# Kernel tuning notes

Hardware: AMD Instinct MI355X
Metric: run time of the kernel (lower is better)

The kernel has to match this reference:

```python
import jax, jax.numpy as jnp
import numpy as np

TAU = 1.0
EPS = 1e-8  # torch cosine_similarity norm clamp


def setup_inputs() -> dict:
    key = jax.random.key(0)
    k1, k2, k3 = jax.random.split(key, 3)
    B, d, M, C = 4096, 128, 8192, 16
    f = jax.random.normal(k1, (B, d), dtype=jnp.float32)
    f_neg = jax.random.normal(k2, (M, d), dtype=jnp.float32)
    labels = jax.random.randint(k3, (B,), 0, C, dtype=jnp.int64)
    return {"f": f, "f_neg": f_neg, "labels": labels, "batch_size": B}


def _normalize(x):
    n = jnp.linalg.norm(x, axis=-1, keepdims=True)
    return x / jnp.maximum(n, EPS)


def reference(f, f_neg, labels, batch_size):
    B = batch_size
    fn = _normalize(f)            # [B, d]
    gn = _normalize(f_neg)        # [M, d]

    sim_bb = jnp.einsum('id,jd->ij', fn, fn)   # [B, B] cosine sims in-batch
    sim_bn = jnp.einsum('id,md->im', fn, gn)   # [B, M] sims with neg bank

    offdiag = ~jnp.eye(B, dtype=bool)                       # exclude self
    pos_mask = (labels[:, None] == labels[None, :]) & offdiag  # [B, B]

    exp_bb = jnp.exp(sim_bb / TAU) * offdiag                # self row removed
    exp_bn = jnp.exp(sim_bn / TAU)
    # denominator_i = sum over all non-self in-batch + all bank negatives
    denom = exp_bb.sum(axis=1) + exp_bn.sum(axis=1)         # [B]

    # -log(exp(s_p/tau)/denom) = log(denom) - s_p/tau, averaged over positives
    neg_log = jnp.log(denom)[:, None] - sim_bb / TAU        # [B, B]
    n_pos = pos_mask.sum(axis=1)                            # [B]
    loss_i = jnp.sum(jnp.where(pos_mask, neg_log, 0.0), axis=1) / n_pos

    return jnp.sum(loss_i) / B  # reduction='mean'
```

## Files before the change

kernel.cpp:

```cpp
#include <hip/hip_runtime.h>
#include <hip/hip_bf16.h>
#include <hip/hip_fp8.h>

#define B_ROWS 4096
#define D_K    128
#define M_ROWS 8192
#define N_TOT  12288
#define NCHUNK 32
#define JT_PER_CHUNK 6
#define JCOLS  64
#define NCLS   16
#define NSTRIPE 32

typedef __attribute__((ext_vector_type(4))) int   intx4;
typedef __attribute__((ext_vector_type(8))) int   intx8;
typedef __attribute__((ext_vector_type(4))) float floatx4;

__device__ __forceinline__ float fp8_to_f32(unsigned char b) {
    __hip_fp8_e4m3 h; h.__x = b; return float(h);
}

__global__ __launch_bounds__(256) void nrm_kernel(
    const float* __restrict__ f, const float* __restrict__ fneg,
    unsigned char* __restrict__ G8, unsigned char* __restrict__ A8,
    float* __restrict__ selfdot, float* __restrict__ expself,
    float* __restrict__ out)
{
    const int tid  = threadIdx.x;
    const int wave = tid >> 6;
    const int lane = tid & 63;
    const int row  = blockIdx.x * 4 + wave;
    if (blockIdx.x == 0 && tid == 0) out[0] = 0.f;
    const float* src = (row < B_ROWS) ? (f + (size_t)row * D_K)
                                      : (fneg + (size_t)(row - B_ROWS) * D_K);
    float2 v = *reinterpret_cast<const float2*>(src + lane * 2);
    float ss = v.x * v.x + v.y * v.y;
    #pragma unroll
    for (int m = 1; m < 64; m <<= 1) ss += __shfl_xor(ss, m, 64);
    const float scale = 1.0f / fmaxf(sqrtf(ss), 1e-8f);
    __hip_fp8_e4m3 q0(v.x * scale);
    __hip_fp8_e4m3 q1(v.y * scale);
    const unsigned short pk =
        (unsigned short)q0.__x | ((unsigned short)q1.__x << 8);
    *reinterpret_cast<unsigned short*>(G8 + (size_t)row * D_K + lane * 2) = pk;
    if (row < B_ROWS) {
        const float s2 = scale * 1.44269504f;
        __hip_fp8_e4m3 a0(v.x * s2);
        __hip_fp8_e4m3 a1(v.y * s2);
        const unsigned short pa =
            (unsigned short)a0.__x | ((unsigned short)a1.__x << 8);
        *reinterpret_cast<unsigned short*>(A8 + (size_t)row * D_K + lane * 2) = pa;
        const float d0 = fp8_to_f32((unsigned char)(pk & 0xff));
        const float d1 = fp8_to_f32((unsigned char)(pk >> 8));
        float sd = d0 * d0 + d1 * d1;
        #pragma unroll
        for (int m = 1; m < 64; m <<= 1) sd += __shfl_xor(sd, m, 64);
        if (lane == 0) {
            selfdot[row] = sd;
            expself[row] = __expf(sd);
        }
    }
}

__global__ __launch_bounds__(256, 2) void sim_kernel(
    const unsigned char* __restrict__ G8, const unsigned char* __restrict__ A8,
    const int* __restrict__ labels, float* __restrict__ part_d,
    float* __restrict__ partS, int* __restrict__ partH)
{
    __shared__ unsigned char Bs[2][JCOLS * D_K];

    const int tid = threadIdx.x;

    if (blockIdx.y >= 32) {
        const int svc    = (blockIdx.y - 32) * NCHUNK + blockIdx.x;
        const int stripe = svc & 31;
        const int dc     = svc >> 5;
        float* Sp = (float*)&Bs[0][0];
        int*   lh = (int*)(Sp + NCLS * 32);
        for (int k = tid; k < NCLS * 32; k += 256) Sp[k] = 0.f;
        if (tid < NCLS) lh[tid] = 0;
        __syncthreads();

        const int j0 = stripe * 128;
        if (dc == 0 && tid < 128) atomicAdd(&lh[labels[j0 + tid]], 1);

        const int d = tid & 31;
        const int w = tid >> 5;
        for (int jj = w; jj < 128; jj += 8) {
            const int j = j0 + jj;
            const int c = labels[j];
            atomicAdd(&Sp[c * 32 + d],
                      fp8_to_f32(G8[(size_t)j * D_K + dc * 32 + d]));
        }
        __syncthreads();
        for (int k = tid; k < NCLS * 32; k += 256) {
            const int c  = k >> 5;
            const int dd = k & 31;
            partS[((size_t)stripe * NCLS + c) * D_K + dc * 32 + dd] = Sp[k];
        }
        if (dc == 0 && tid < NCLS) partH[stripe * NCLS + tid] = lh[tid];
        return;
    }

    const int jc   = blockIdx.x;
    const int it   = blockIdx.y;
    const int wave = tid >> 6;
    const int lane = tid & 63;
    const int i0   = it * 128 + wave * 32;

    const int r16 = lane & 15;
    const int grp = lane >> 4;

    const unsigned char* Abase = A8 + (size_t)(i0 + r16) * D_K + grp * 32;
    intx8 afr[2];
    #pragma unroll
    for (int a = 0; a < 2; ++a)
        afr[a] = *reinterpret_cast<const intx8*>(Abase + (size_t)a * 16 * D_K);

    float dsum[2][4];
    #pragma unroll
    for (int a = 0; a < 2; ++a)
        #pragma unroll
        for (int r = 0; r < 4; ++r) dsum[a][r] = 0.f;

    int srcoff[2];
    #pragma unroll
    for (int s = 0; s < 2; ++s) {
        const int row  = s * 32 + (tid >> 3);
        const int gran = (tid & 7) ^ ((row >> 2) & 1);
        srcoff[s] = row * D_K + gran * 16;
    }

    intx4 streg[2];
    {
        const unsigned char* src =
            G8 + (size_t)(jc * JT_PER_CHUNK) * JCOLS * D_K;
        #pragma unroll
        for (int s = 0; s < 2; ++s)
            streg[s] = *reinterpret_cast<const intx4*>(src + srcoff[s]);
        #pragma unroll
        for (int s = 0; s < 2; ++s)
            *reinterpret_cast<intx4*>(&Bs[0][0] + s * 4096 + tid * 16) =
                streg[s];
    }

    for (int t = 0; t < JT_PER_CHUNK; ++t) {
        const int cur = t & 1;
        __syncthreads();

        if (t + 1 < JT_PER_CHUNK) {
            const unsigned char* src =
                G8 + (size_t)(jc * JT_PER_CHUNK + t + 1) * JCOLS * D_K;
            #pragma unroll
            for (int s = 0; s < 2; ++s)
                streg[s] = *reinterpret_cast<const intx4*>(src + srcoff[s]);
        }

        floatx4 acc[2][4];
        #pragma unroll
        for (int a = 0; a < 2; ++a)
            #pragma unroll
            for (int b = 0; b < 4; ++b)
                acc[a][b] = (floatx4){0.f, 0.f, 0.f, 0.f};

        const unsigned char* base = &Bs[cur][0];
        #pragma unroll
        for (int b = 0; b < 4; ++b) {
            const int jloc = b * 16 + r16;
            const int sw   = (jloc >> 2) & 1;
            intx4 lo = *reinterpret_cast<const intx4*>(
                base + jloc * D_K + ((2 * grp)     ^ sw) * 16);
            intx4 hi = *reinterpret_cast<const intx4*>(
                base + jloc * D_K + ((2 * grp + 1) ^ sw) * 16);
            intx8 bfr;
            if (sw) { intx4 tmp = lo; lo = hi; hi = tmp; }
            #pragma unroll
            for (int e = 0; e < 4; ++e) { bfr[e] = lo[e]; bfr[e + 4] = hi[e]; }
            #pragma unroll
            for (int a = 0; a < 2; ++a)
                acc[a][b] = __builtin_amdgcn_mfma_scale_f32_16x16x128_f8f6f4(
                    afr[a], bfr, acc[a][b], 0, 0,
                    0, 0x7F7F7F7F, 0, 0x7F7F7F7F);
        }

        #pragma unroll
        for (int a = 0; a < 2; ++a)
            #pragma unroll
            for (int r = 0; r < 4; ++r) {
                float s0 = exp2f(acc[a][0][r]) + exp2f(acc[a][1][r]);
                float s1 = exp2f(acc[a][2][r]) + exp2f(acc[a][3][r]);
                dsum[a][r] += s0 + s1;
            }

        if (t + 1 < JT_PER_CHUNK) {
            #pragma unroll
            for (int s = 0; s < 2; ++s)
                *reinterpret_cast<intx4*>(
                    &Bs[cur ^ 1][0] + s * 4096 + tid * 16) = streg[s];
        }
    }

    #pragma unroll
    for (int a = 0; a < 2; ++a)
        #pragma unroll
        for (int r = 0; r < 4; ++r) {
            #pragma unroll
            for (int m = 1; m < 16; m <<= 1)
                dsum[a][r] += __shfl_xor(dsum[a][r], m, 64);
        }
    if (r16 == 0) {
        #pragma unroll
        for (int a = 0; a < 2; ++a)
            #pragma unroll
            for (int r = 0; r < 4; ++r)
                part_d[(size_t)(i0 + a * 16 + grp * 4 + r) * NCHUNK + jc] =
                    dsum[a][r];
    }
}

__global__ __launch_bounds__(256) void fin_kernel(
    const float* __restrict__ part_d, const float* __restrict__ partS,
    const int* __restrict__ partH, const int* __restrict__ labels,
    const float* __restrict__ selfdot, const float* __restrict__ expself,
    float* __restrict__ out)
{
    const int tid  = threadIdx.x;
    const int wave = tid >> 6;
    const int lane = tid & 63;

    if (blockIdx.x >= 256) {
        const int c = blockIdx.x - 256;
        __shared__ float SpC[4][D_K];
        __shared__ float wt[4];

        float tc = 0.f;
        for (int i = tid; i < B_ROWS; i += 256)
            tc += (labels[i] == c) ? selfdot[i] : 0.f;
        #pragma unroll
        for (int m = 1; m < 64; m <<= 1) tc += __shfl_xor(tc, m, 64);
        if (lane == 0) wt[wave] = tc;

        const int d0 = lane * 2;
        float s0 = 0.f, s1 = 0.f;
        for (int s = wave; s < NSTRIPE; s += 4) {
            float2 p = *reinterpret_cast<const float2*>(
                partS + ((size_t)s * NCLS + c) * D_K + d0);
            s0 += p.x; s1 += p.y;
        }
        SpC[wave][d0]     = s0;
        SpC[wave][d0 + 1] = s1;
        __syncthreads();

        if (wave == 0) {
            const float v0 = SpC[0][d0] + SpC[1][d0] + SpC[2][d0] + SpC[3][d0];
            const float v1 = SpC[0][d0 + 1] + SpC[1][d0 + 1]
                           + SpC[2][d0 + 1] + SpC[3][d0 + 1];
            float dsq = v0 * v0 + v1 * v1;
            float hf = (lane < NSTRIPE)
                ? (float)partH[lane * NCLS + c] : 0.f;
            #pragma unroll
            for (int m = 1; m < 64; m <<= 1) {
                dsq += __shfl_xor(dsq, m, 64);
                hf  += __shfl_xor(hf, m, 64);
            }
            if (lane == 0) {
                const float Tc = wt[0] + wt[1] + wt[2] + wt[3];
                const int   h  = (int)hf;
                if (h > 1)
                    atomicAdd(out, -((dsq - Tc) / (float)(h - 1))
                                      * (1.0f / (float)B_ROWS));
            }
        }
        return;
    }

    __shared__ float w4[4];
    const int i0 = (blockIdx.x * 4 + wave) * 4;
    float pd[4];
    #pragma unroll
    for (int r = 0; r < 4; ++r)
        pd[r] = (lane < NCHUNK)
            ? part_d[(size_t)(i0 + r) * NCHUNK + lane] : 0.f;
    float es[4];
    #pragma unroll
    for (int r = 0; r < 4; ++r) es[r] = expself[i0 + r];

    #pragma unroll
    for (int r = 0; r < 4; ++r) {
        #pragma unroll
        for (int m = 1; m < 32; m <<= 1)
            pd[r] += __shfl_xor(pd[r], m, 64);
    }
    if (lane == 0) {
        float lsum = 0.f;
        #pragma unroll
        for (int r = 0; r < 4; ++r)
            lsum += __logf(pd[r] - es[r]);
        w4[wave] = lsum;
    }
    __syncthreads();
    if (tid == 0)
        atomicAdd(out, (w4[0] + w4[1] + w4[2] + w4[3]) * (1.0f / (float)B_ROWS));
}

extern "C" void kernel_launch(void* const* d_in, const int* in_sizes, int n_in,
                              void* d_out, int out_size, void* d_ws, size_t ws_size,
                              hipStream_t stream) {
    const float* f      = (const float*)d_in[0];
    const float* fneg   = (const float*)d_in[1];
    const int*   labels = (const int*)d_in[2];
    float*       out    = (float*)d_out;

    char* ws = (char*)d_ws;
    unsigned char* G8      = (unsigned char*)(ws);
    unsigned char* A8      = (unsigned char*)(ws + 1572864);
    float*         part_d  = (float*)(ws + 2097152);
    float*         partS   = (float*)(ws + 2621440);
    int*           partH   = (int*)(ws + 2883584);
    float*         selfdot = (float*)(ws + 2885632);
    float*         expself = (float*)(ws + 2902016);

    nrm_kernel<<<N_TOT / 4, 256, 0, stream>>>(f, fneg, G8, A8, selfdot,
                                              expself, out);

    dim3 gridS(NCHUNK, 36);
    sim_kernel<<<gridS, 256, 0, stream>>>(G8, A8, labels, part_d, partS, partH);

    fin_kernel<<<272, 256, 0, stream>>>(part_d, partS, partH, labels,
                                        selfdot, expself, out);
}
```

Measured before the change: 39.99 us.

## Repartition class-sum blocks into 128 row stripes and schedule them first

The per-class feature sum blocks now each take 32 rows across all 128 dims, giving 128 stripes instead of 32 stripes split by dim chunk. Each thread loads 16 bytes with a single vector load and does 16 shared atomics. The class-sum blocks are moved to the low blockIdx.y values so they are dispatched before the similarity blocks. The cost is a larger partS buffer (128 stripes), a longer reduction in the finalize kernel, and more shared-atomic contention on the 16 class rows.

```diff
diff --git a/kernel.cpp b/kernel.cpp
--- a/kernel.cpp
+++ b/kernel.cpp
@@ -10,7 +10,7 @@
 #define JT_PER_CHUNK 6
 #define JCOLS  64
 #define NCLS   16
-#define NSTRIPE 32
+#define NSTRIPE 128
 
 typedef __attribute__((ext_vector_type(4))) int   intx4;
 typedef __attribute__((ext_vector_type(8))) int   intx8;
@@ -71,39 +71,37 @@
 
     const int tid = threadIdx.x;
 
-    if (blockIdx.y >= 32) {
-        const int svc    = (blockIdx.y - 32) * NCHUNK + blockIdx.x;
-        const int stripe = svc & 31;
-        const int dc     = svc >> 5;
+    if (blockIdx.y < 4) {
+        const int svc = blockIdx.y * NCHUNK + blockIdx.x;
         float* Sp = (float*)&Bs[0][0];
-        int*   lh = (int*)(Sp + NCLS * 32);
-        for (int k = tid; k < NCLS * 32; k += 256) Sp[k] = 0.f;
+        int*   lh = (int*)(Sp + NCLS * D_K);
+        for (int k = tid; k < NCLS * D_K; k += 256) Sp[k] = 0.f;
         if (tid < NCLS) lh[tid] = 0;
         __syncthreads();
 
-        const int j0 = stripe * 128;
-        if (dc == 0 && tid < 128) atomicAdd(&lh[labels[j0 + tid]], 1);
-
-        const int d = tid & 31;
-        const int w = tid >> 5;
-        for (int jj = w; jj < 128; jj += 8) {
-            const int j = j0 + jj;
-            const int c = labels[j];
-            atomicAdd(&Sp[c * 32 + d],
-                      fp8_to_f32(G8[(size_t)j * D_K + dc * 32 + d]));
-        }
+        const int j0   = svc * 32;
+        const int rloc = tid >> 3;
+        const int slot = tid & 7;
+        const int j    = j0 + rloc;
+        const int c    = labels[j];
+        const intx4 v  = *reinterpret_cast<const intx4*>(
+            G8 + (size_t)j * D_K + slot * 16);
+        const unsigned char* vb = (const unsigned char*)&v;
+        #pragma unroll
+        for (int k = 0; k < 16; ++k)
+            atomicAdd(&Sp[c * D_K + slot * 16 + k], fp8_to_f32(vb[k]));
+        if (tid < 32) atomicAdd(&lh[labels[j0 + tid]], 1);
         __syncthreads();
-        for (int k = tid; k < NCLS * 32; k += 256) {
-            const int c  = k >> 5;
-            const int dd = k & 31;
-            partS[((size_t)stripe * NCLS + c) * D_K + dc * 32 + dd] = Sp[k];
-        }
-        if (dc == 0 && tid < NCLS) partH[stripe * NCLS + tid] = lh[tid];
+
+        #pragma unroll
+        for (int k = 0; k < 8; ++k)
+            partS[(size_t)svc * (NCLS * D_K) + tid * 8 + k] = Sp[tid * 8 + k];
+        if (tid < NCLS) partH[svc * NCLS + tid] = lh[tid];
         return;
     }
 
     const int jc   = blockIdx.x;
-    const int it   = blockIdx.y;
+    const int it   = blockIdx.y - 4;
     const int wave = tid >> 6;
     const int lane = tid & 63;
     const int i0   = it * 128 + wave * 32;
@@ -256,8 +254,8 @@
             const float v1 = SpC[0][d0 + 1] + SpC[1][d0 + 1]
                            + SpC[2][d0 + 1] + SpC[3][d0 + 1];
             float dsq = v0 * v0 + v1 * v1;
-            float hf = (lane < NSTRIPE)
-                ? (float)partH[lane * NCLS + c] : 0.f;
+            float hf = (float)partH[lane * NCLS + c]
+                     + (float)partH[(lane + 64) * NCLS + c];
             #pragma unroll
             for (int m = 1; m < 64; m <<= 1) {
                 dsq += __shfl_xor(dsq, m, 64);
@@ -316,9 +314,9 @@
     unsigned char* A8      = (unsigned char*)(ws + 1572864);
     float*         part_d  = (float*)(ws + 2097152);
     float*         partS   = (float*)(ws + 2621440);
-    int*           partH   = (int*)(ws + 2883584);
-    float*         selfdot = (float*)(ws + 2885632);
-    float*         expself = (float*)(ws + 2902016);
+    int*           partH   = (int*)(ws + 3670016);
+    float*         selfdot = (float*)(ws + 3678208);
+    float*         expself = (float*)(ws + 3694592);
 
     nrm_kernel<<<N_TOT / 4, 256, 0, stream>>>(f, fneg, G8, A8, selfdot,
                                               expself, out);
```

New measurement: 52.10 us. 1.3x slower.
